# Performance work log

Measured on AMD Instinct MI355X. Metric: run time of the kernel, lower is better.

Reference implementation:

```python
import jax, jax.numpy as jnp
import numpy as np

B, S, D, H = 2, 2048, 1024, 16
DH = D // H


def setup_inputs() -> dict:
    key = jax.random.key(0)
    ks = jax.random.split(key, 12)
    f = lambda k, sh: jax.random.normal(k, sh, dtype=jnp.float32)
    inp = {"q": f(ks[0], (B, S, D)), "k": f(ks[1], (B, S, D)), "v": f(ks[2], (B, S, D))}
    scale = 1.0 / np.sqrt(D)
    names = ["q", "k", "v", "o"]
    for i, n in enumerate(names):
        inp["W" + n] = f(ks[3 + i], (D, D)) * scale
        inp["b" + n] = f(ks[7 + i], (D,)) * scale
    # causal mask: True = masked out
    inp["mask"] = jnp.triu(jnp.ones((S, S), dtype=bool), k=1)[None, None]
    return inp


def _rope(x):
    # x: [b, h, s, dh]; non-standard RoPE from AbsPositionEncoding
    s, dh = x.shape[2], x.shape[3]
    inv = jnp.exp(jnp.arange(0, dh, 2, dtype=jnp.float32) * (-(4.0 * jnp.log(jnp.float32(10.0))) / dh))
    pos = jnp.arange(s, dtype=jnp.float32)[:, None]
    sin = jnp.sin(pos * inv)  # [s, dh/2]
    cos = jnp.cos(pos * inv)
    x1 = x[..., 0::2]
    x2 = x[..., 1::2]
    out = jnp.stack([x1 * sin - x2 * cos, -x1 * cos - x2 * sin], axis=-1)
    return out.reshape(x.shape)


def reference(q, k, v, Wq, bq, Wk, bk, Wv, bv, Wo, bo, mask):
    b, s, d = q.shape
    h, dh = H, DH

    def proj(x, W, bias):
        return (x @ W.T + bias).reshape(b, -1, h, dh).transpose(0, 2, 1, 3)

    Q = proj(q, Wq, bq)
    K = proj(k, Wk, bk)
    V = proj(v, Wv, bv)
    PQ = _rope(Q)
    PK = _rope(K)
    # NOTE: source's forward() path applies NO 1/sqrt(dh) scaling
    scores = jnp.einsum('bhqd,bhkd->bhqk', PQ, PK)
    neg = jnp.finfo(scores.dtype).min
    scores = jnp.where(mask, neg, scores)
    p = jax.nn.softmax(scores, axis=-1)
    p = jnp.where(mask, jnp.float32(0.0), p)
    out = jnp.einsum('bhqk,bhkd->bhqd', p, V)
    out = out.transpose(0, 2, 1, 3).reshape(b, s, d)
    return out @ Wo.T + bo
```

## Files before the change

kernel.cpp:

```cpp
#include <hip/hip_runtime.h>
#include <stdint.h>

#define BB 2
#define SS 2048
#define DD 1024
#define HH 16
#define DH 64
#define MM 4096
#define NQTB 16

typedef __attribute__((ext_vector_type(8))) short short8;
typedef __attribute__((ext_vector_type(4))) float floatx4;
typedef __attribute__((ext_vector_type(16))) float floatx16;
typedef unsigned short u16;

#define MFMA16(a,b,c) __builtin_amdgcn_mfma_f32_16x16x32_bf16((a),(b),(c),0,0,0)
#define MFMA32(a,b,c) __builtin_amdgcn_mfma_f32_32x32x16_bf16((a),(b),(c),0,0,0)

__device__ __forceinline__ u16 f2bf(float f) {
  unsigned u = __float_as_uint(f);
  u += 0x7fffu + ((u >> 16) & 1u);
  return (u16)(u >> 16);
}

__device__ __forceinline__ unsigned cvtpk(float lo, float hi2) {
  unsigned r;
  asm("v_cvt_pk_bf16_f32 %0, %1, %2" : "=v"(r) : "v"(lo), "v"(hi2));
  return r;
}

__device__ __forceinline__ void gll16(const void* g, void* l) {
  __builtin_amdgcn_global_load_lds((const __attribute__((address_space(1))) void*)g,
                                   (__attribute__((address_space(3))) void*)l,
                                   16, 0, 0);
}

__global__ __launch_bounds__(256) void sincos_k(float2* __restrict__ tab) {
  const int t = blockIdx.x * 256 + threadIdx.x;
  const int s = t >> 5, j = t & 31;
  const float inv = expf(-(float)j * (0.125f * 2.302585092994046f));
  const float a = (float)s * inv;
  tab[t] = make_float2(sinf(a), cosf(a));
}

__global__ __launch_bounds__(256) void conv_qkv(const float* __restrict__ a, const float* __restrict__ b,
                                                const float* __restrict__ c,
                                                u16* __restrict__ oa, u16* __restrict__ ob, u16* __restrict__ oc) {
  const float* s = blockIdx.y == 0 ? a : (blockIdx.y == 1 ? b : c);
  u16* d = blockIdx.y == 0 ? oa : (blockIdx.y == 1 ? ob : oc);
  const int i = (blockIdx.x * 256 + threadIdx.x) * 4;
  const float4 x = *(const float4*)(s + i);
  ushort4 p; p.x = f2bf(x.x); p.y = f2bf(x.y); p.z = f2bf(x.z); p.w = f2bf(x.w);
  *(ushort4*)(d + i) = p;
}

__global__ __launch_bounds__(256) void conv_w(const float* __restrict__ a, const float* __restrict__ b,
                                              const float* __restrict__ c, const float* __restrict__ d4,
                                              u16* __restrict__ oa, u16* __restrict__ ob,
                                              u16* __restrict__ oc, u16* __restrict__ od) {
  const float* s = blockIdx.y == 0 ? a : (blockIdx.y == 1 ? b : (blockIdx.y == 2 ? c : d4));
  u16* d = blockIdx.y == 0 ? oa : (blockIdx.y == 1 ? ob : (blockIdx.y == 2 ? oc : od));
  const int i = (blockIdx.x * 256 + threadIdx.x) * 4;
  const float4 x = *(const float4*)(s + i);
  ushort4 p; p.x = f2bf(x.x); p.y = f2bf(x.y); p.z = f2bf(x.z); p.w = f2bf(x.w);
  *(ushort4*)(d + i) = p;
}

__device__ __forceinline__ void gemm_body(const u16* __restrict__ A, const u16* __restrict__ Bt,
                                          const float* __restrict__ bias, float* __restrict__ C,
                                          int M, int N, int K, u16* As, u16* Bs) {
  const int tid = threadIdx.x;
  const int w = tid >> 6, l = tid & 63;
  const int lr = l & 15, lq = l >> 4;
  const int m0 = blockIdx.y * 128, n0 = blockIdx.x * 128;
  const int wm = (w >> 1) * 64, wn = (w & 1) * 64;

  floatx4 acc[4][4];
#pragma unroll
  for (int i = 0; i < 4; ++i)
#pragma unroll
    for (int j = 0; j < 4; ++j) acc[i][j] = (floatx4){0.f, 0.f, 0.f, 0.f};

  const int srow = w * 32 + (l >> 2);
  const int scol = (l & 3) * 8;
  const u16* ag = A + (size_t)(m0 + srow) * K + scol;
  const u16* bg = Bt + (size_t)(n0 + srow) * K + scol;
  u16* as0 = &As[w * 1024];
  u16* bs0 = &Bs[w * 1024];

  for (int k0 = 0; k0 < K; k0 += 32) {
    gll16(ag + k0, as0);
    gll16(ag + (size_t)16 * K + k0, as0 + 512);
    gll16(bg + k0, bs0);
    gll16(bg + (size_t)16 * K + k0, bs0 + 512);
    __syncthreads();
    short8 af[4], bfv[4];
#pragma unroll
    for (int i = 0; i < 4; ++i) af[i] = *(const short8*)&As[(wm + i * 16 + lr) * 32 + lq * 8];
#pragma unroll
    for (int j = 0; j < 4; ++j) bfv[j] = *(const short8*)&Bs[(wn + j * 16 + lr) * 32 + lq * 8];
    __builtin_amdgcn_s_setprio(1);
#pragma unroll
    for (int i = 0; i < 4; ++i)
#pragma unroll
      for (int j = 0; j < 4; ++j) acc[i][j] = MFMA16(af[i], bfv[j], acc[i][j]);
    __builtin_amdgcn_s_setprio(0);
    __syncthreads();
  }

#pragma unroll
  for (int i = 0; i < 4; ++i) {
    const int row = m0 + wm + i * 16 + lq * 4;
#pragma unroll
    for (int j = 0; j < 4; ++j) {
      const int col = n0 + wn + j * 16 + lr;
      const float bv = bias[col];
      float* cp = C + (size_t)row * N + col;
#pragma unroll
      for (int r = 0; r < 4; ++r) cp[(size_t)r * N] = acc[i][j][r] + bv;
    }
  }
}

__global__ __launch_bounds__(256) void gemm_bt(const u16* __restrict__ A, const u16* __restrict__ Bt,
                                               const float* __restrict__ bias, float* __restrict__ C,
                                               int M, int N, int K) {
  __shared__ alignas(16) u16 As[128 * 32];
  __shared__ alignas(16) u16 Bs[128 * 32];
  gemm_body(A, Bt, bias, C, M, N, K, As, Bs);
}

__global__ __launch_bounds__(256) void gemm3(const u16* __restrict__ A0, const u16* __restrict__ A1, const u16* __restrict__ A2,
                                             const u16* __restrict__ B0, const u16* __restrict__ B1, const u16* __restrict__ B2,
                                             const float* __restrict__ c0, const float* __restrict__ c1, const float* __restrict__ c2,
                                             float* __restrict__ C0, float* __restrict__ C1, float* __restrict__ C2) {
  __shared__ alignas(16) u16 As[128 * 32];
  __shared__ alignas(16) u16 Bs[128 * 32];
  const int z = blockIdx.z;
  const u16* A = z == 0 ? A0 : (z == 1 ? A1 : A2);
  const u16* Bt = z == 0 ? B0 : (z == 1 ? B1 : B2);
  const float* bias = z == 0 ? c0 : (z == 1 ? c1 : c2);
  float* C = z == 0 ? C0 : (z == 1 ? C1 : C2);
  gemm_body(A, Bt, bias, C, MM, DD, DD, As, Bs);
}

__global__ __launch_bounds__(256) void rope_post(const float* __restrict__ Qlin, const float* __restrict__ Klin,
                                                 const float2* __restrict__ tab,
                                                 u16* __restrict__ Qo, u16* __restrict__ Ko) {
  const int t = blockIdx.x * 256 + threadIdx.x;
  const int j = t & 31;
  const int h = (t >> 5) & 15;
  const int row = t >> 9;
  const int s = row & (SS - 1);
  const int b = row >> 11;
  const float* src = blockIdx.z ? Klin : Qlin;
  u16* dst = blockIdx.z ? Ko : Qo;
  const float2 x = *(const float2*)(src + (size_t)row * DD + h * 64 + 2 * j);
  const float2 sc = tab[s * 32 + j];
  const float e = x.x * sc.x - x.y * sc.y;
  const float o = -x.x * sc.y - x.y * sc.x;
  const size_t oi = ((size_t)(b * HH + h) * SS + s) * DH + 2 * j;
  ushort2 pk; pk.x = f2bf(e); pk.y = f2bf(o);
  *(ushort2*)(dst + oi) = pk;
}

__global__ __launch_bounds__(256) void v_post(const float* __restrict__ Vlin, u16* __restrict__ Vt) {
  __shared__ alignas(16) u16 tile[64][72];
  const int s0 = blockIdx.x * 64;
  const int bh = blockIdx.y;
  const int b = bh >> 4, h = bh & 15;
  const int t = threadIdx.x;
  const int sr = t >> 4;
  const int e4 = (t & 15) * 4;
#pragma unroll
  for (int it = 0; it < 4; ++it) {
    const int srow = sr + it * 16;
    const float4 x = *(const float4*)(Vlin + ((size_t)(b * SS + s0 + srow)) * DD + h * 64 + e4);
    tile[e4 + 0][srow] = f2bf(x.x);
    tile[e4 + 1][srow] = f2bf(x.y);
    tile[e4 + 2][srow] = f2bf(x.z);
    tile[e4 + 3][srow] = f2bf(x.w);
  }
  __syncthreads();
  const int e = t >> 2;
  const int sc = (t & 3) * 16;
  u16* op = Vt + ((size_t)bh * DH + e) * SS + s0 + sc;
  *(short8*)op = *(const short8*)&tile[e][sc];
  *(short8*)(op + 8) = *(const short8*)&tile[e][sc + 8];
}

__global__ __launch_bounds__(256) void attn_fwd(const u16* __restrict__ Qr, const u16* __restrict__ Kr,
                                                const u16* __restrict__ Vt, u16* __restrict__ O) {
  __shared__ alignas(16) u16 Ks[2][64 * 64];
  __shared__ alignas(16) u16 Vs[2][64 * 64];
  const int bid = blockIdx.x;
  const int qt = (NQTB - 1) - (bid >> 5);
  const int bh = bid & 31;
  const int w = threadIdx.x >> 6, l = threadIdx.x & 63;
  const int ql = l & 31, hi = l >> 5;
  const int qw0 = qt * 128 + w * 32;
  const u16* Qh = Qr + (size_t)bh * SS * DH;
  const u16* Kh = Kr + (size_t)bh * SS * DH;
  const u16* Vh = Vt + (size_t)bh * DH * SS;

  short8 qf[4];
#pragma unroll
  for (int i = 0; i < 4; ++i)
    qf[i] = *(const short8*)(Qh + (size_t)(qw0 + ql) * DH + i * 16 + hi * 8);

  floatx16 oacc[2];
#pragma unroll
  for (int dt = 0; dt < 2; ++dt)
#pragma unroll
    for (int r = 0; r < 16; ++r) oacc[dt][r] = 0.f;
  float mrun = -1e30f, lrun = 0.f;

  const int srow = w * 16 + (l >> 3);
  const int sgofs = ((((l & 7) * 16) ^ (((l >> 3) & 7) << 4)) >> 1);
  const int swzb = (ql & 7) << 4;

#define STAGE(buf, kv0)                                                                  \
  do {                                                                                   \
    gll16(Kh + (size_t)((kv0) + srow) * DH + sgofs,       &Ks[buf][(w * 16) * 64]);      \
    gll16(Kh + (size_t)((kv0) + srow + 8) * DH + sgofs,   &Ks[buf][(w * 16 + 8) * 64]);  \
    gll16(Vh + (size_t)srow * SS + (kv0) + sgofs,         &Vs[buf][(w * 16) * 64]);      \
    gll16(Vh + (size_t)(srow + 8) * SS + (kv0) + sgofs,   &Vs[buf][(w * 16 + 8) * 64]);  \
  } while (0)

  const int T = 2 * qt + 2;
  STAGE(0, 0);
  __syncthreads();

  for (int t = 0; t < T; ++t) {
    const int cur = t & 1;
    if (t < T - 1) STAGE(cur ^ 1, (t + 1) * 64);
    const int kv0 = t * 64;

    if (kv0 <= qw0 + 31) {
      floatx16 st[2];
#pragma unroll
      for (int tt = 0; tt < 2; ++tt)
#pragma unroll
        for (int r = 0; r < 16; ++r) st[tt][r] = 0.f;
      __builtin_amdgcn_s_setprio(1);
#pragma unroll
      for (int tt = 0; tt < 2; ++tt)
#pragma unroll
        for (int i = 0; i < 4; ++i) {
          const u16* kp = &Ks[cur][(tt * 32 + ql) * 64 + (((32 * i + 16 * hi) ^ swzb) >> 1)];
          st[tt] = MFMA32(*(const short8*)kp, qf[i], st[tt]);
        }
      __builtin_amdgcn_s_setprio(0);

      if (kv0 + 63 > qw0) {
#pragma unroll
        for (int tt = 0; tt < 2; ++tt)
#pragma unroll
          for (int r = 0; r < 16; ++r) {
            const int kv = kv0 + tt * 32 + (r & 3) + 8 * (r >> 2) + 4 * hi;
            if (kv > qw0 + ql) st[tt][r] = -1e30f;
          }
      }

      floatx16 mx;
#pragma unroll
      for (int r = 0; r < 16; ++r) mx[r] = fmaxf(st[0][r], st[1][r]);
      float m8[8];
#pragma unroll
      for (int r = 0; r < 8; ++r) m8[r] = fmaxf(mx[r], mx[r + 8]);
      float m4a = fmaxf(m8[0], m8[4]), m4b = fmaxf(m8[1], m8[5]);
      float m4c = fmaxf(m8[2], m8[6]), m4d = fmaxf(m8[3], m8[7]);
      float tmax = fmaxf(fmaxf(m4a, m4b), fmaxf(m4c, m4d));
      tmax = fmaxf(tmax, __shfl_xor(tmax, 32));
      const float mn = fmaxf(mrun, tmax);
      const float sc = __expf(mrun - mn);
      mrun = mn;
      float ps = 0.f;
#pragma unroll
      for (int tt = 0; tt < 2; ++tt)
#pragma unroll
        for (int r = 0; r < 16; ++r) {
          const float p = __expf(st[tt][r] - mn);
          st[tt][r] = p;
          ps += p;
        }
      ps += __shfl_xor(ps, 32);
      lrun = lrun * sc + ps;
#pragma unroll
      for (int dt = 0; dt < 2; ++dt)
#pragma unroll
        for (int r = 0; r < 16; ++r) oacc[dt][r] *= sc;

      short8 pfrag[4];
#pragma unroll
      for (int c = 0; c < 4; ++c) {
        const int tt = c >> 1;
        const int A0 = 2 * (c & 1), A1 = A0 + 1;
        const unsigned P00 = cvtpk(st[tt][4 * A0 + 0], st[tt][4 * A0 + 1]);
        const unsigned P01 = cvtpk(st[tt][4 * A0 + 2], st[tt][4 * A0 + 3]);
        const unsigned P10 = cvtpk(st[tt][4 * A1 + 0], st[tt][4 * A1 + 1]);
        const unsigned P11 = cvtpk(st[tt][4 * A1 + 2], st[tt][4 * A1 + 3]);
        const unsigned S0 = hi ? P00 : P10;
        const unsigned S1 = hi ? P01 : P11;
        const unsigned R0 = (unsigned)__shfl_xor((int)S0, 32);
        const unsigned R1 = (unsigned)__shfl_xor((int)S1, 32);
        union { unsigned u[4]; short8 s; } fd;
        fd.u[0] = hi ? R0 : P00;
        fd.u[1] = hi ? R1 : P01;
        fd.u[2] = hi ? P10 : R0;
        fd.u[3] = hi ? P11 : R1;
        pfrag[c] = fd.s;
      }

      __builtin_amdgcn_s_setprio(1);
#pragma unroll
      for (int dt = 0; dt < 2; ++dt)
#pragma unroll
        for (int c = 0; c < 4; ++c) {
          const u16* vp = &Vs[cur][(dt * 32 + ql) * 64 + (((32 * c + 16 * hi) ^ swzb) >> 1)];
          oacc[dt] = MFMA32(*(const short8*)vp, pfrag[c], oacc[dt]);
        }
      __builtin_amdgcn_s_setprio(0);
    }
    __syncthreads();
  }
#undef STAGE

  const float inv = 1.0f / lrun;
  const int b = bh >> 4, h = bh & 15;
  u16* orow = O + ((size_t)(b * SS + qw0 + ql)) * DD + h * DH;
#pragma unroll
  for (int dt = 0; dt < 2; ++dt)
#pragma unroll
    for (int g = 0; g < 4; ++g) {
      ushort4 pk;
      pk.x = f2bf(oacc[dt][4 * g + 0] * inv);
      pk.y = f2bf(oacc[dt][4 * g + 1] * inv);
      pk.z = f2bf(oacc[dt][4 * g + 2] * inv);
      pk.w = f2bf(oacc[dt][4 * g + 3] * inv);
      *(ushort4*)(orow + dt * 32 + 8 * g + 4 * hi) = pk;
    }
}

extern "C" void kernel_launch(void* const* d_in, const int* in_sizes, int n_in,
                              void* d_out, int out_size, void* d_ws, size_t ws_size,
                              hipStream_t stream) {
  (void)in_sizes; (void)n_in; (void)out_size; (void)ws_size;
  const float* q  = (const float*)d_in[0];
  const float* k  = (const float*)d_in[1];
  const float* v  = (const float*)d_in[2];
  const float* Wq = (const float*)d_in[3];
  const float* bq = (const float*)d_in[4];
  const float* Wk = (const float*)d_in[5];
  const float* bk = (const float*)d_in[6];
  const float* Wv = (const float*)d_in[7];
  const float* bv = (const float*)d_in[8];
  const float* Wo = (const float*)d_in[9];
  const float* bo = (const float*)d_in[10];
  float* out = (float*)d_out;

  char* ws = (char*)d_ws;
  size_t off = 0;
  auto carve = [&](size_t bytes) { char* p = ws + off; off += (bytes + 255) & ~(size_t)255; return p; };
  u16* qb   = (u16*)carve((size_t)MM * DD * 2);
  u16* kb   = (u16*)carve((size_t)MM * DD * 2);
  u16* vb   = (u16*)carve((size_t)MM * DD * 2);
  u16* wqb  = (u16*)carve((size_t)DD * DD * 2);
  u16* wkb  = (u16*)carve((size_t)DD * DD * 2);
  u16* wvb  = (u16*)carve((size_t)DD * DD * 2);
  u16* wob  = (u16*)carve((size_t)DD * DD * 2);
  float* Qlin = (float*)carve((size_t)MM * DD * 4);
  float* Klin = (float*)carve((size_t)MM * DD * 4);
  float* Vlin = (float*)carve((size_t)MM * DD * 4);
  u16* Vtr  = (u16*)carve((size_t)MM * DD * 2);
  float2* tab = (float2*)carve((size_t)SS * 32 * 8);
  u16* Qro = qb;
  u16* Kro = kb;
  u16* Ob  = vb;

  sincos_k<<<SS * 32 / 256, 256, 0, stream>>>(tab);
  conv_qkv<<<dim3(MM * DD / 1024, 3), 256, 0, stream>>>(q, k, v, qb, kb, vb);
  conv_w<<<dim3(DD * DD / 1024, 4), 256, 0, stream>>>(Wq, Wk, Wv, Wo, wqb, wkb, wvb, wob);
  gemm3<<<dim3(DD / 128, MM / 128, 3), 256, 0, stream>>>(qb, kb, vb, wqb, wkb, wvb,
                                                         bq, bk, bv, Qlin, Klin, Vlin);
  rope_post<<<dim3(MM * DD / 2 / 256, 1, 2), 256, 0, stream>>>(Qlin, Klin, tab, Qro, Kro);
  v_post<<<dim3(SS / 64, BB * HH), 256, 0, stream>>>(Vlin, Vtr);
  attn_fwd<<<NQTB * BB * HH, 256, 0, stream>>>(Qro, Kro, Vtr, Ob);
  gemm_bt<<<dim3(DD / 128, MM / 128), 256, 0, stream>>>(Ob, wob, bo, out, MM, DD, DD);
}
```

Before: 278.7 us.

## Fuse RoPE and V transpose into QKV GEMM epilogue, shrink GEMM and attention tiles

Folds the bias, RoPE rotation and bf16 conversion for Q/K, and the V transpose, into the QKV projection GEMM epilogue. This removes the fp32 intermediate buffers and the separate rope_post and v_post kernels. GEMM tiles shrink from 128x128 to 64x128 to launch more blocks. Attention switches to 64-query tiles with 128 threads, doubling the grid, and drops the per-tile skip branch. The epilogue now does scattered 2-byte stores with shuffles, and each K/V tile is reused by fewer queries.

```diff
diff --git a/kernel.cpp b/kernel.cpp
--- a/kernel.cpp
+++ b/kernel.cpp
@@ -7,7 +7,6 @@
 #define HH 16
 #define DH 64
 #define MM 4096
-#define NQTB 16
 
 typedef __attribute__((ext_vector_type(8))) short short8;
 typedef __attribute__((ext_vector_type(4))) float floatx4;
@@ -66,139 +65,149 @@
   *(ushort4*)(d + i) = p;
 }
 
-__device__ __forceinline__ void gemm_body(const u16* __restrict__ A, const u16* __restrict__ Bt,
-                                          const float* __restrict__ bias, float* __restrict__ C,
-                                          int M, int N, int K, u16* As, u16* Bs) {
+__device__ __forceinline__ void gemm_core64(const u16* __restrict__ A, const u16* __restrict__ Bt,
+                                            int K, u16* As, u16* Bs, floatx4 acc[2][4],
+                                            int m0, int n0) {
   const int tid = threadIdx.x;
   const int w = tid >> 6, l = tid & 63;
   const int lr = l & 15, lq = l >> 4;
-  const int m0 = blockIdx.y * 128, n0 = blockIdx.x * 128;
-  const int wm = (w >> 1) * 64, wn = (w & 1) * 64;
-
-  floatx4 acc[4][4];
-#pragma unroll
-  for (int i = 0; i < 4; ++i)
+  const int wm = (w >> 1) * 32, wn = (w & 1) * 64;
+
+#pragma unroll
+  for (int i = 0; i < 2; ++i)
 #pragma unroll
     for (int j = 0; j < 4; ++j) acc[i][j] = (floatx4){0.f, 0.f, 0.f, 0.f};
 
-  const int srow = w * 32 + (l >> 2);
+  const int arow = w * 16 + (l >> 2);
+  const int brow = w * 32 + (l >> 2);
   const int scol = (l & 3) * 8;
-  const u16* ag = A + (size_t)(m0 + srow) * K + scol;
-  const u16* bg = Bt + (size_t)(n0 + srow) * K + scol;
-  u16* as0 = &As[w * 1024];
+  const u16* ag = A + (size_t)(m0 + arow) * K + scol;
+  const u16* bg = Bt + (size_t)(n0 + brow) * K + scol;
+  u16* as0 = &As[w * 512];
   u16* bs0 = &Bs[w * 1024];
 
   for (int k0 = 0; k0 < K; k0 += 32) {
     gll16(ag + k0, as0);
-    gll16(ag + (size_t)16 * K + k0, as0 + 512);
     gll16(bg + k0, bs0);
     gll16(bg + (size_t)16 * K + k0, bs0 + 512);
     __syncthreads();
-    short8 af[4], bfv[4];
-#pragma unroll
-    for (int i = 0; i < 4; ++i) af[i] = *(const short8*)&As[(wm + i * 16 + lr) * 32 + lq * 8];
+    short8 af[2], bfv[4];
+#pragma unroll
+    for (int i = 0; i < 2; ++i) af[i] = *(const short8*)&As[(wm + i * 16 + lr) * 32 + lq * 8];
 #pragma unroll
     for (int j = 0; j < 4; ++j) bfv[j] = *(const short8*)&Bs[(wn + j * 16 + lr) * 32 + lq * 8];
     __builtin_amdgcn_s_setprio(1);
 #pragma unroll
-    for (int i = 0; i < 4; ++i)
+    for (int i = 0; i < 2; ++i)
 #pragma unroll
       for (int j = 0; j < 4; ++j) acc[i][j] = MFMA16(af[i], bfv[j], acc[i][j]);
     __builtin_amdgcn_s_setprio(0);
     __syncthreads();
   }
-
-#pragma unroll
-  for (int i = 0; i < 4; ++i) {
-    const int row = m0 + wm + i * 16 + lq * 4;
-#pragma unroll
-    for (int j = 0; j < 4; ++j) {
-      const int col = n0 + wn + j * 16 + lr;
-      const float bv = bias[col];
-      float* cp = C + (size_t)row * N + col;
-#pragma unroll
-      for (int r = 0; r < 4; ++r) cp[(size_t)r * N] = acc[i][j][r] + bv;
-    }
-  }
-}
-
-__global__ __launch_bounds__(256) void gemm_bt(const u16* __restrict__ A, const u16* __restrict__ Bt,
-                                               const float* __restrict__ bias, float* __restrict__ C,
-                                               int M, int N, int K) {
-  __shared__ alignas(16) u16 As[128 * 32];
-  __shared__ alignas(16) u16 Bs[128 * 32];
-  gemm_body(A, Bt, bias, C, M, N, K, As, Bs);
-}
-
-__global__ __launch_bounds__(256) void gemm3(const u16* __restrict__ A0, const u16* __restrict__ A1, const u16* __restrict__ A2,
-                                             const u16* __restrict__ B0, const u16* __restrict__ B1, const u16* __restrict__ B2,
-                                             const float* __restrict__ c0, const float* __restrict__ c1, const float* __restrict__ c2,
-                                             float* __restrict__ C0, float* __restrict__ C1, float* __restrict__ C2) {
-  __shared__ alignas(16) u16 As[128 * 32];
+}
+
+__global__ __launch_bounds__(256) void gemm3_fused(
+    const u16* __restrict__ A0, const u16* __restrict__ A1, const u16* __restrict__ A2,
+    const u16* __restrict__ B0, const u16* __restrict__ B1, const u16* __restrict__ B2,
+    const float* __restrict__ c0, const float* __restrict__ c1, const float* __restrict__ c2,
+    u16* __restrict__ Qro, u16* __restrict__ Kro, u16* __restrict__ Vtr,
+    const float2* __restrict__ tab) {
+  __shared__ alignas(16) u16 As[64 * 32];
   __shared__ alignas(16) u16 Bs[128 * 32];
   const int z = blockIdx.z;
   const u16* A = z == 0 ? A0 : (z == 1 ? A1 : A2);
   const u16* Bt = z == 0 ? B0 : (z == 1 ? B1 : B2);
   const float* bias = z == 0 ? c0 : (z == 1 ? c1 : c2);
-  float* C = z == 0 ? C0 : (z == 1 ? C1 : C2);
-  gemm_body(A, Bt, bias, C, MM, DD, DD, As, Bs);
-}
-
-__global__ __launch_bounds__(256) void rope_post(const float* __restrict__ Qlin, const float* __restrict__ Klin,
-                                                 const float2* __restrict__ tab,
-                                                 u16* __restrict__ Qo, u16* __restrict__ Ko) {
-  const int t = blockIdx.x * 256 + threadIdx.x;
-  const int j = t & 31;
-  const int h = (t >> 5) & 15;
-  const int row = t >> 9;
-  const int s = row & (SS - 1);
-  const int b = row >> 11;
-  const float* src = blockIdx.z ? Klin : Qlin;
-  u16* dst = blockIdx.z ? Ko : Qo;
-  const float2 x = *(const float2*)(src + (size_t)row * DD + h * 64 + 2 * j);
-  const float2 sc = tab[s * 32 + j];
-  const float e = x.x * sc.x - x.y * sc.y;
-  const float o = -x.x * sc.y - x.y * sc.x;
-  const size_t oi = ((size_t)(b * HH + h) * SS + s) * DH + 2 * j;
-  ushort2 pk; pk.x = f2bf(e); pk.y = f2bf(o);
-  *(ushort2*)(dst + oi) = pk;
-}
-
-__global__ __launch_bounds__(256) void v_post(const float* __restrict__ Vlin, u16* __restrict__ Vt) {
-  __shared__ alignas(16) u16 tile[64][72];
-  const int s0 = blockIdx.x * 64;
-  const int bh = blockIdx.y;
-  const int b = bh >> 4, h = bh & 15;
-  const int t = threadIdx.x;
-  const int sr = t >> 4;
-  const int e4 = (t & 15) * 4;
-#pragma unroll
-  for (int it = 0; it < 4; ++it) {
-    const int srow = sr + it * 16;
-    const float4 x = *(const float4*)(Vlin + ((size_t)(b * SS + s0 + srow)) * DD + h * 64 + e4);
-    tile[e4 + 0][srow] = f2bf(x.x);
-    tile[e4 + 1][srow] = f2bf(x.y);
-    tile[e4 + 2][srow] = f2bf(x.z);
-    tile[e4 + 3][srow] = f2bf(x.w);
+  const int m0 = blockIdx.y * 64, n0 = blockIdx.x * 128;
+
+  floatx4 acc[2][4];
+  gemm_core64(A, Bt, DD, As, Bs, acc, m0, n0);
+
+  const int tid = threadIdx.x;
+  const int w = tid >> 6, l = tid & 63;
+  const int lr = l & 15, lq = l >> 4;
+  const int wm = (w >> 1) * 32, wn = (w & 1) * 64;
+
+  if (z == 2) {
+#pragma unroll
+    for (int i = 0; i < 2; ++i) {
+      const int row = m0 + wm + i * 16 + lq * 4;
+      const int b = row >> 11, s = row & (SS - 1);
+#pragma unroll
+      for (int j = 0; j < 4; ++j) {
+        const int col = n0 + wn + j * 16 + lr;
+        const int h = col >> 6, e = col & 63;
+        const float bv = bias[col];
+        ushort4 pk;
+        pk.x = f2bf(acc[i][j][0] + bv);
+        pk.y = f2bf(acc[i][j][1] + bv);
+        pk.z = f2bf(acc[i][j][2] + bv);
+        pk.w = f2bf(acc[i][j][3] + bv);
+        *(ushort4*)(Vtr + ((size_t)(b * HH + h) * DH + e) * SS + s) = pk;
+      }
+    }
+  } else {
+    u16* dst = z ? Kro : Qro;
+#pragma unroll
+    for (int i = 0; i < 2; ++i) {
+#pragma unroll
+      for (int j = 0; j < 4; ++j) {
+        const int col = n0 + wn + j * 16 + lr;
+        const int h = col >> 6, e = col & 63;
+        const float bv = bias[col];
+#pragma unroll
+        for (int r = 0; r < 4; ++r) {
+          const int row = m0 + wm + i * 16 + lq * 4 + r;
+          const int b = row >> 11, s = row & (SS - 1);
+          const float v = acc[i][j][r] + bv;
+          const float p = __shfl_xor(v, 1);
+          const float2 sc = tab[s * 32 + (e >> 1)];
+          const float ov = ((e & 1) == 0) ? (v * sc.x - p * sc.y)
+                                          : (-p * sc.y - v * sc.x);
+          dst[((size_t)(b * HH + h) * SS + s) * DH + e] = f2bf(ov);
+        }
+      }
+    }
   }
-  __syncthreads();
-  const int e = t >> 2;
-  const int sc = (t & 3) * 16;
-  u16* op = Vt + ((size_t)bh * DH + e) * SS + s0 + sc;
-  *(short8*)op = *(const short8*)&tile[e][sc];
-  *(short8*)(op + 8) = *(const short8*)&tile[e][sc + 8];
-}
-
-__global__ __launch_bounds__(256) void attn_fwd(const u16* __restrict__ Qr, const u16* __restrict__ Kr,
+}
+
+__global__ __launch_bounds__(256) void gemm_bt(const u16* __restrict__ A, const u16* __restrict__ Bt,
+                                               const float* __restrict__ bias, float* __restrict__ C,
+                                               int M, int N, int K) {
+  __shared__ alignas(16) u16 As[64 * 32];
+  __shared__ alignas(16) u16 Bs[128 * 32];
+  const int m0 = blockIdx.y * 64, n0 = blockIdx.x * 128;
+  floatx4 acc[2][4];
+  gemm_core64(A, Bt, K, As, Bs, acc, m0, n0);
+
+  const int tid = threadIdx.x;
+  const int w = tid >> 6, l = tid & 63;
+  const int lr = l & 15, lq = l >> 4;
+  const int wm = (w >> 1) * 32, wn = (w & 1) * 64;
+#pragma unroll
+  for (int i = 0; i < 2; ++i) {
+    const int row = m0 + wm + i * 16 + lq * 4;
+#pragma unroll
+    for (int j = 0; j < 4; ++j) {
+      const int col = n0 + wn + j * 16 + lr;
+      const float bv = bias[col];
+      float* cp = C + (size_t)row * N + col;
+#pragma unroll
+      for (int r = 0; r < 4; ++r) cp[(size_t)r * N] = acc[i][j][r] + bv;
+    }
+  }
+}
+
+__global__ __launch_bounds__(128) void attn_fwd(const u16* __restrict__ Qr, const u16* __restrict__ Kr,
                                                 const u16* __restrict__ Vt, u16* __restrict__ O) {
   __shared__ alignas(16) u16 Ks[2][64 * 64];
   __shared__ alignas(16) u16 Vs[2][64 * 64];
   const int bid = blockIdx.x;
-  const int qt = (NQTB - 1) - (bid >> 5);
+  const int qt = 31 - (bid >> 5);
   const int bh = bid & 31;
   const int w = threadIdx.x >> 6, l = threadIdx.x & 63;
   const int ql = l & 31, hi = l >> 5;
-  const int qw0 = qt * 128 + w * 32;
+  const int qw0 = qt * 64 + w * 32;
   const u16* Qh = Qr + (size_t)bh * SS * DH;
   const u16* Kh = Kr + (size_t)bh * SS * DH;
   const u16* Vh = Vt + (size_t)bh * DH * SS;
@@ -215,19 +224,23 @@
     for (int r = 0; r < 16; ++r) oacc[dt][r] = 0.f;
   float mrun = -1e30f, lrun = 0.f;
 
-  const int srow = w * 16 + (l >> 3);
+  const int srow = w * 32 + (l >> 3);
   const int sgofs = ((((l & 7) * 16) ^ (((l >> 3) & 7) << 4)) >> 1);
   const int swzb = (ql & 7) << 4;
 
-#define STAGE(buf, kv0)                                                                  \
-  do {                                                                                   \
-    gll16(Kh + (size_t)((kv0) + srow) * DH + sgofs,       &Ks[buf][(w * 16) * 64]);      \
-    gll16(Kh + (size_t)((kv0) + srow + 8) * DH + sgofs,   &Ks[buf][(w * 16 + 8) * 64]);  \
-    gll16(Vh + (size_t)srow * SS + (kv0) + sgofs,         &Vs[buf][(w * 16) * 64]);      \
-    gll16(Vh + (size_t)(srow + 8) * SS + (kv0) + sgofs,   &Vs[buf][(w * 16 + 8) * 64]);  \
+#define STAGE(buf, kv0)                                                                    \
+  do {                                                                                     \
+    gll16(Kh + (size_t)((kv0) + srow) * DH + sgofs,        &Ks[buf][(w * 32) * 64]);       \
+    gll16(Kh + (size_t)((kv0) + srow + 8) * DH + sgofs,    &Ks[buf][(w * 32 + 8) * 64]);   \
+    gll16(Kh + (size_t)((kv0) + srow + 16) * DH + sgofs,   &Ks[buf][(w * 32 + 16) * 64]);  \
+    gll16(Kh + (size_t)((kv0) + srow + 24) * DH + sgofs,   &Ks[buf][(w * 32 + 24) * 64]);  \
+    gll16(Vh + (size_t)srow * SS + (kv0) + sgofs,          &Vs[buf][(w * 32) * 64]);       \
+    gll16(Vh + (size_t)(srow + 8) * SS + (kv0) + sgofs,    &Vs[buf][(w * 32 + 8) * 64]);   \
+    gll16(Vh + (size_t)(srow + 16) * SS + (kv0) + sgofs,   &Vs[buf][(w * 32 + 16) * 64]);  \
+    gll16(Vh + (size_t)(srow + 24) * SS + (kv0) + sgofs,   &Vs[buf][(w * 32 + 24) * 64]);  \
   } while (0)
 
-  const int T = 2 * qt + 2;
+  const int T = qt + 1;
   STAGE(0, 0);
   __syncthreads();
 
@@ -236,92 +249,91 @@
     if (t < T - 1) STAGE(cur ^ 1, (t + 1) * 64);
     const int kv0 = t * 64;
 
-    if (kv0 <= qw0 + 31) {
-      floatx16 st[2];
+    floatx16 st[2];
+#pragma unroll
+    for (int tt = 0; tt < 2; ++tt)
+#pragma unroll
+      for (int r = 0; r < 16; ++r) st[tt][r] = 0.f;
+    __builtin_amdgcn_s_setprio(1);
+#pragma unroll
+    for (int tt = 0; tt < 2; ++tt)
+#pragma unroll
+      for (int i = 0; i < 4; ++i) {
+        const u16* kp = &Ks[cur][(tt * 32 + ql) * 64 + (((32 * i + 16 * hi) ^ swzb) >> 1)];
+        st[tt] = MFMA32(*(const short8*)kp, qf[i], st[tt]);
+      }
+    __builtin_amdgcn_s_setprio(0);
+
+    if (t == T - 1) {
 #pragma unroll
       for (int tt = 0; tt < 2; ++tt)
 #pragma unroll
-        for (int r = 0; r < 16; ++r) st[tt][r] = 0.f;
-      __builtin_amdgcn_s_setprio(1);
-#pragma unroll
-      for (int tt = 0; tt < 2; ++tt)
-#pragma unroll
-        for (int i = 0; i < 4; ++i) {
-          const u16* kp = &Ks[cur][(tt * 32 + ql) * 64 + (((32 * i + 16 * hi) ^ swzb) >> 1)];
-          st[tt] = MFMA32(*(const short8*)kp, qf[i], st[tt]);
+        for (int r = 0; r < 16; ++r) {
+          const int kv = kv0 + tt * 32 + (r & 3) + 8 * (r >> 2) + 4 * hi;
+          if (kv > qw0 + ql) st[tt][r] = -1e30f;
         }
-      __builtin_amdgcn_s_setprio(0);
-
-      if (kv0 + 63 > qw0) {
-#pragma unroll
-        for (int tt = 0; tt < 2; ++tt)
-#pragma unroll
-          for (int r = 0; r < 16; ++r) {
-            const int kv = kv0 + tt * 32 + (r & 3) + 8 * (r >> 2) + 4 * hi;
-            if (kv > qw0 + ql) st[tt][r] = -1e30f;
-          }
-      }
-
-      floatx16 mx;
-#pragma unroll
-      for (int r = 0; r < 16; ++r) mx[r] = fmaxf(st[0][r], st[1][r]);
-      float m8[8];
-#pragma unroll
-      for (int r = 0; r < 8; ++r) m8[r] = fmaxf(mx[r], mx[r + 8]);
-      float m4a = fmaxf(m8[0], m8[4]), m4b = fmaxf(m8[1], m8[5]);
-      float m4c = fmaxf(m8[2], m8[6]), m4d = fmaxf(m8[3], m8[7]);
-      float tmax = fmaxf(fmaxf(m4a, m4b), fmaxf(m4c, m4d));
-      tmax = fmaxf(tmax, __shfl_xor(tmax, 32));
-      const float mn = fmaxf(mrun, tmax);
-      const float sc = __expf(mrun - mn);
-      mrun = mn;
-      float ps = 0.f;
-#pragma unroll
-      for (int tt = 0; tt < 2; ++tt)
-#pragma unroll
-        for (int r = 0; r < 16; ++r) {
-          const float p = __expf(st[tt][r] - mn);
-          st[tt][r] = p;
-          ps += p;
-        }
-      ps += __shfl_xor(ps, 32);
-      lrun = lrun * sc + ps;
-#pragma unroll
-      for (int dt = 0; dt < 2; ++dt)
-#pragma unroll
-        for (int r = 0; r < 16; ++r) oacc[dt][r] *= sc;
-
-      short8 pfrag[4];
+    }
+
+    floatx16 mx;
+#pragma unroll
+    for (int r = 0; r < 16; ++r) mx[r] = fmaxf(st[0][r], st[1][r]);
+    float m8[8];
+#pragma unroll
+    for (int r = 0; r < 8; ++r) m8[r] = fmaxf(mx[r], mx[r + 8]);
+    float m4a = fmaxf(m8[0], m8[4]), m4b = fmaxf(m8[1], m8[5]);
+    float m4c = fmaxf(m8[2], m8[6]), m4d = fmaxf(m8[3], m8[7]);
+    float tmax = fmaxf(fmaxf(m4a, m4b), fmaxf(m4c, m4d));
+    tmax = fmaxf(tmax, __shfl_xor(tmax, 32));
+
+    const float mn = fmaxf(mrun, tmax);
+    const float sc = __expf(mrun - mn);
+    mrun = mn;
+    float ps = 0.f;
+#pragma unroll
+    for (int tt = 0; tt < 2; ++tt)
+#pragma unroll
+      for (int r = 0; r < 16; ++r) {
+        const float p = __expf(st[tt][r] - mn);
+        st[tt][r] = p;
+        ps += p;
+      }
+    ps += __shfl_xor(ps, 32);
+    lrun = lrun * sc + ps;
+#pragma unroll
+    for (int dt = 0; dt < 2; ++dt)
+#pragma unroll
+      for (int r = 0; r < 16; ++r) oacc[dt][r] *= sc;
+
+    short8 pfrag[4];
+#pragma unroll
+    for (int c = 0; c < 4; ++c) {
+      const int tt = c >> 1;
+      const int A0r = 2 * (c & 1), A1r = A0r + 1;
+      const unsigned P00 = cvtpk(st[tt][4 * A0r + 0], st[tt][4 * A0r + 1]);
+      const unsigned P01 = cvtpk(st[tt][4 * A0r + 2], st[tt][4 * A0r + 3]);
+      const unsigned P10 = cvtpk(st[tt][4 * A1r + 0], st[tt][4 * A1r + 1]);
+      const unsigned P11 = cvtpk(st[tt][4 * A1r + 2], st[tt][4 * A1r + 3]);
+      const unsigned S0 = hi ? P00 : P10;
+      const unsigned S1 = hi ? P01 : P11;
+      const unsigned R0 = (unsigned)__shfl_xor((int)S0, 32);
+      const unsigned R1 = (unsigned)__shfl_xor((int)S1, 32);
+      union { unsigned u[4]; short8 s; } fd;
+      fd.u[0] = hi ? R0 : P00;
+      fd.u[1] = hi ? R1 : P01;
+      fd.u[2] = hi ? P10 : R0;
+      fd.u[3] = hi ? P11 : R1;
+      pfrag[c] = fd.s;
+    }
+
+    __builtin_amdgcn_s_setprio(1);
+#pragma unroll
+    for (int dt = 0; dt < 2; ++dt)
 #pragma unroll
       for (int c = 0; c < 4; ++c) {
-        const int tt = c >> 1;
-        const int A0 = 2 * (c & 1), A1 = A0 + 1;
-        const unsigned P00 = cvtpk(st[tt][4 * A0 + 0], st[tt][4 * A0 + 1]);
-        const unsigned P01 = cvtpk(st[tt][4 * A0 + 2], st[tt][4 * A0 + 3]);
-        const unsigned P10 = cvtpk(st[tt][4 * A1 + 0], st[tt][4 * A1 + 1]);
-        const unsigned P11 = cvtpk(st[tt][4 * A1 + 2], st[tt][4 * A1 + 3]);
-        const unsigned S0 = hi ? P00 : P10;
-        const unsigned S1 = hi ? P01 : P11;
-        const unsigned R0 = (unsigned)__shfl_xor((int)S0, 32);
-        const unsigned R1 = (unsigned)__shfl_xor((int)S1, 32);
-        union { unsigned u[4]; short8 s; } fd;
-        fd.u[0] = hi ? R0 : P00;
-        fd.u[1] = hi ? R1 : P01;
-        fd.u[2] = hi ? P10 : R0;
-        fd.u[3] = hi ? P11 : R1;
-        pfrag[c] = fd.s;
-      }
-
-      __builtin_amdgcn_s_setprio(1);
-#pragma unroll
-      for (int dt = 0; dt < 2; ++dt)
-#pragma unroll
-        for (int c = 0; c < 4; ++c) {
-          const u16* vp = &Vs[cur][(dt * 32 + ql) * 64 + (((32 * c + 16 * hi) ^ swzb) >> 1)];
-          oacc[dt] = MFMA32(*(const short8*)vp, pfrag[c], oacc[dt]);
-        }
-      __builtin_amdgcn_s_setprio(0);
-    }
+        const u16* vp = &Vs[cur][(dt * 32 + ql) * 64 + (((32 * c + 16 * hi) ^ swzb) >> 1)];
+        oacc[dt] = MFMA32(*(const short8*)vp, pfrag[c], oacc[dt]);
+      }
+    __builtin_amdgcn_s_setprio(0);
     __syncthreads();
   }
 #undef STAGE
@@ -369,22 +381,17 @@
   u16* wkb  = (u16*)carve((size_t)DD * DD * 2);
   u16* wvb  = (u16*)carve((size_t)DD * DD * 2);
   u16* wob  = (u16*)carve((size_t)DD * DD * 2);
-  float* Qlin = (float*)carve((size_t)MM * DD * 4);
-  float* Klin = (float*)carve((size_t)MM * DD * 4);
-  float* Vlin = (float*)carve((size_t)MM * DD * 4);
+  u16* Qro  = (u16*)carve((size_t)MM * DD * 2);
+  u16* Kro  = (u16*)carve((size_t)MM * DD * 2);
   u16* Vtr  = (u16*)carve((size_t)MM * DD * 2);
   float2* tab = (float2*)carve((size_t)SS * 32 * 8);
-  u16* Qro = qb;
-  u16* Kro = kb;
-  u16* Ob  = vb;
+  u16* Ob = qb;
 
   sincos_k<<<SS * 32 / 256, 256, 0, stream>>>(tab);
   conv_qkv<<<dim3(MM * DD / 1024, 3), 256, 0, stream>>>(q, k, v, qb, kb, vb);
   conv_w<<<dim3(DD * DD / 1024, 4), 256, 0, stream>>>(Wq, Wk, Wv, Wo, wqb, wkb, wvb, wob);
-  gemm3<<<dim3(DD / 128, MM / 128, 3), 256, 0, stream>>>(qb, kb, vb, wqb, wkb, wvb,
-                                                         bq, bk, bv, Qlin, Klin, Vlin);
-  rope_post<<<dim3(MM * DD / 2 / 256, 1, 2), 256, 0, stream>>>(Qlin, Klin, tab, Qro, Kro);
-  v_post<<<dim3(SS / 64, BB * HH), 256, 0, stream>>>(Vlin, Vtr);
-  attn_fwd<<<NQTB * BB * HH, 256, 0, stream>>>(Qro, Kro, Vtr, Ob);
-  gemm_bt<<<dim3(DD / 128, MM / 128), 256, 0, stream>>>(Ob, wob, bo, out, MM, DD, DD);
-}
+  gemm3_fused<<<dim3(DD / 128, MM / 64, 3), 256, 0, stream>>>(qb, kb, vb, wqb, wkb, wvb,
+                                                              bq, bk, bv, Qro, Kro, Vtr, tab);
+  attn_fwd<<<32 * BB * HH, 128, 0, stream>>>(Qro, Kro, Vtr, Ob);
+  gemm_bt<<<dim3(DD / 128, MM / 64), 256, 0, stream>>>(Ob, wob, bo, out, MM, DD, DD);
+}
```

After: 269.1 us. -3.5%, faster.
